# Performance work log

Measured on AMD Instinct MI355X. Metric: run time of the kernel, lower is better.

Reference implementation:

```python
import jax, jax.numpy as jnp
import numpy as np

D_K = 64
NEG_INF = -1.0e9


def setup_inputs() -> dict:
    key = jax.random.key(0)
    kq, kk, kv = jax.random.split(key, 3)
    B, H, S, D = 2, 16, 2048, D_K
    Q = jax.random.normal(kq, (B, H, S, D), dtype=jnp.float32)
    K = jax.random.normal(kk, (B, H, S, D), dtype=jnp.float32)
    V = jax.random.normal(kv, (B, H, S, D), dtype=jnp.float32)
    # causal mask: True where attention is DISALLOWED (strict upper triangle)
    attn_mask = jnp.triu(jnp.ones((S, S), dtype=bool), k=1)
    return {"Q": Q, "K": K, "V": V, "attn_mask": attn_mask}


def reference(Q, K, V, attn_mask):
    # scores = Q @ (K / sqrt(d_k))^T  -> [B,H,S,S]
    scale = 1.0 / np.sqrt(D_K).astype(np.float32)
    scores = jnp.einsum("bhqd,bhkd->bhqk", Q, K * scale)
    scores = jnp.where(attn_mask, NEG_INF, scores)  # masked_fill_(mask, -1e9)
    attn = jax.nn.softmax(scores, axis=-1)
    context = jnp.einsum("bhqk,bhkd->bhqd", attn, V)
    return (context, attn)
```

## Files before the change

kernel.cpp:

```cpp
#include <hip/hip_runtime.h>

constexpr int S_LEN = 2048;
constexpr int D_K   = 64;
constexpr int N_BH  = 32;
constexpr int KB    = 64;

typedef __attribute__((ext_vector_type(8))) short short8;
typedef __attribute__((ext_vector_type(4))) float f32x4;
typedef unsigned short ushort_t;

__device__ __forceinline__ unsigned short f2bf(float f) {
    unsigned int u = __builtin_bit_cast(unsigned int, f);
    u += 0x7fffu + ((u >> 16) & 1u);
    return (unsigned short)(u >> 16);
}
__device__ __forceinline__ float bf2f(unsigned short h) {
    unsigned int u = ((unsigned int)h) << 16;
    return __builtin_bit_cast(float, u);
}

__global__ __launch_bounds__(256)
void prep_k(const float* __restrict__ K, ushort_t* __restrict__ Kws) {
    const int idx = blockIdx.x * 256 + threadIdx.x;
    const float4* src = (const float4*)K + (size_t)idx * 2;
    float4 a = src[0], b = src[1];
    float x[8] = {a.x, a.y, a.z, a.w, b.x, b.y, b.z, b.w};
    short8 o;
    #pragma unroll
    for (int j = 0; j < 8; ++j) o[j] = (short)f2bf(x[j] * 0.125f);
    *(short8*)(Kws + (size_t)idx * 8) = o;
}

__global__ __launch_bounds__(256)
void prep_v(const float* __restrict__ V, ushort_t* __restrict__ Vws) {
    const int gid = blockIdx.x * 256 + threadIdx.x;
    const int u   = gid & 511;
    const int bc  = gid >> 9;
    const int c   = bc & 31;
    const int bh  = bc >> 5;
    const int kg  = u >> 6;
    const int d   = u & 63;
    const float* vp = V + ((size_t)bh * S_LEN + c * KB + kg * 8) * D_K + d;
    short8 o;
    #pragma unroll
    for (int i = 0; i < 8; ++i) o[i] = (short)f2bf(vp[(size_t)i * D_K]);
    *(short8*)(Vws + ((size_t)(bh * 32 + c) * D_K + d) * KB + kg * 8) = o;
}

__global__ __launch_bounds__(256, 4)
void sdpa_main(const float* __restrict__ Q, const ushort_t* __restrict__ Kws,
               const ushort_t* __restrict__ Vws, float* __restrict__ out)
{
    __shared__ __align__(16) ushort_t Kbuf[2][4096];
    __shared__ __align__(16) ushort_t Vbuf[2][4096];
    __shared__ __align__(16) ushort_t Plds[4][1024];

    const int tid = threadIdx.x;
    const int w   = tid >> 6;
    const int l   = tid & 63;
    const int lr  = l & 15;
    const int lh  = l >> 4;

    const int bx  = blockIdx.x;
    const int g   = bx >> 8;
    const int idx = bx & 255;
    const int bh  = idx >> 3;
    const int r   = idx & 7;
    int t;
    switch (g) {
        case 0:  t = 31 - r; break;
        case 1:  t = 16 + r; break;
        case 2:  t = 15 - r; break;
        default: t = r;      break;
    }
    const int nch = t + 1;
    const int q0  = t * 64;
    const int qg_base = q0 + w * 16 + lh * 4;

    float* ctx_out  = out;
    float* attn_out = out + (size_t)N_BH * S_LEN * D_K;

    const short8* Kt  = (const short8*)(Kws + (size_t)bh * S_LEN * D_K);
    const short8* Vt8 = (const short8*)(Vws + (size_t)bh * 32 * 4096);

    const int wrow0  = tid >> 3;
    const int wcol   = (tid & 7) << 4;
    const int wphys0 = wrow0 * 128 + (wcol ^ ((wrow0 & 7) << 4));
    const int wphys1 = wphys0 + 32 * 128;
    const int rsw    = (lr & 7) << 4;

    short8 qhi[2], qlo[2];
    {
        const float* qrow = Q + ((size_t)bh * S_LEN + q0 + w * 16 + lr) * D_K;
        #pragma unroll
        for (int ds = 0; ds < 2; ++ds) {
            const float4* p4 = (const float4*)(qrow + ds * 32 + lh * 8);
            float4 a = p4[0], bq = p4[1];
            float x[8] = {a.x, a.y, a.z, a.w, bq.x, bq.y, bq.z, bq.w};
            short8 hi, lo;
            #pragma unroll
            for (int j = 0; j < 8; ++j) {
                unsigned short h = f2bf(x[j]);
                hi[j] = (short)h;
                lo[j] = (short)f2bf(x[j] - bf2f(h));
            }
            qhi[ds] = hi; qlo[ds] = lo;
        }
    }

    float inv_[4];
    {
        float sum[4] = {0.f, 0.f, 0.f, 0.f};

        auto p1 = [&](const char* Kb, int c) {
            #pragma unroll
            for (int nt = 0; nt < 4; ++nt) {
                f32x4 acc = {0.f, 0.f, 0.f, 0.f};
                #pragma unroll
                for (int ks = 0; ks < 2; ++ks) {
                    short8 bk = *(const short8*)(Kb + (nt * 16 + lr) * 128 + ((ks * 64 + lh * 16) ^ rsw));
                    acc = __builtin_amdgcn_mfma_f32_16x16x32_bf16(qhi[ks], bk, acc, 0, 0, 0);
                }
                const int kg = c * KB + nt * 16 + lr;
                #pragma unroll
                for (int rr = 0; rr < 4; ++rr)
                    if (kg <= qg_base + rr) sum[rr] += __expf(fminf(acc[rr], 60.f));
            }
        };

        short8 kE0 = Kt[tid], kE1 = Kt[tid + 256];
        *(short8*)((char*)&Kbuf[0][0] + wphys0) = kE0;
        *(short8*)((char*)&Kbuf[0][0] + wphys1) = kE1;
        short8 kO0 = Kt[512 + tid], kO1 = Kt[512 + tid + 256];
        __syncthreads();
        for (int c = 0; c < nch; c += 2) {
            if (c + 2 < nch) { kE0 = Kt[(c + 2) * 512 + tid]; kE1 = Kt[(c + 2) * 512 + tid + 256]; }
            p1((const char*)&Kbuf[0][0], c);
            if (c + 1 < nch) {
                *(short8*)((char*)&Kbuf[1][0] + wphys0) = kO0;
                *(short8*)((char*)&Kbuf[1][0] + wphys1) = kO1;
            }
            __syncthreads();
            if (c + 1 < nch) {
                if (c + 3 < nch) { kO0 = Kt[(c + 3) * 512 + tid]; kO1 = Kt[(c + 3) * 512 + tid + 256]; }
                p1((const char*)&Kbuf[1][0], c + 1);
                if (c + 2 < nch) {
                    *(short8*)((char*)&Kbuf[0][0] + wphys0) = kE0;
                    *(short8*)((char*)&Kbuf[0][0] + wphys1) = kE1;
                }
                __syncthreads();
            }
        }
        #pragma unroll
        for (int rr = 0; rr < 4; ++rr) {
            float s = sum[rr];
            s += __shfl_xor(s, 1);
            s += __shfl_xor(s, 2);
            s += __shfl_xor(s, 4);
            s += __shfl_xor(s, 8);
            inv_[rr] = 1.f / s;
        }
    }

    f32x4 ctx[4];
    #pragma unroll
    for (int nt = 0; nt < 4; ++nt) ctx[nt] = (f32x4){0.f, 0.f, 0.f, 0.f};

    {
        auto p2 = [&](const char* Kb, const char* Vb, int c) {
            #pragma unroll
            for (int nt = 0; nt < 4; ++nt) {
                f32x4 acc = {0.f, 0.f, 0.f, 0.f};
                #pragma unroll
                for (int ks = 0; ks < 2; ++ks) {
                    short8 bk = *(const short8*)(Kb + (nt * 16 + lr) * 128 + ((ks * 64 + lh * 16) ^ rsw));
                    acc = __builtin_amdgcn_mfma_f32_16x16x32_bf16(qhi[ks], bk, acc, 0, 0, 0);
                    acc = __builtin_amdgcn_mfma_f32_16x16x32_bf16(qlo[ks], bk, acc, 0, 0, 0);
                }
                const int kg = c * KB + nt * 16 + lr;
                #pragma unroll
                for (int rr = 0; rr < 4; ++rr) {
                    const int pwr = lh * 4 + rr;
                    const int qg  = qg_base + rr;
                    float p = (kg <= qg) ? __expf(fminf(acc[rr], 60.f)) * inv_[rr] : 0.f;
                    attn_out[((size_t)bh * S_LEN + qg) * S_LEN + kg] = p;
                    Plds[w][pwr * 64 + ((nt * 16 + lr) ^ ((pwr & 7) << 3))] = f2bf(p);
                }
            }
            #pragma unroll
            for (int ks = 0; ks < 2; ++ks) {
                short8 pa = *(const short8*)&Plds[w][lr * 64 + ((ks * 32 + lh * 8) ^ ((lr & 7) << 3))];
                #pragma unroll
                for (int nt = 0; nt < 4; ++nt) {
                    short8 vb = *(const short8*)(Vb + (nt * 16 + lr) * 128 + ((ks * 64 + lh * 16) ^ rsw));
                    ctx[nt] = __builtin_amdgcn_mfma_f32_16x16x32_bf16(pa, vb, ctx[nt], 0, 0, 0);
                }
            }
        };

        short8 kE0 = Kt[tid],        kE1 = Kt[tid + 256];
        short8 vE0 = Vt8[tid],       vE1 = Vt8[tid + 256];
        *(short8*)((char*)&Kbuf[0][0] + wphys0) = kE0;
        *(short8*)((char*)&Kbuf[0][0] + wphys1) = kE1;
        *(short8*)((char*)&Vbuf[0][0] + wphys0) = vE0;
        *(short8*)((char*)&Vbuf[0][0] + wphys1) = vE1;
        short8 kO0 = Kt[512 + tid],  kO1 = Kt[512 + tid + 256];
        short8 vO0 = Vt8[512 + tid], vO1 = Vt8[512 + tid + 256];
        __syncthreads();
        for (int c = 0; c < nch; c += 2) {
            if (c + 2 < nch) {
                kE0 = Kt[(c + 2) * 512 + tid];  kE1 = Kt[(c + 2) * 512 + tid + 256];
                vE0 = Vt8[(c + 2) * 512 + tid]; vE1 = Vt8[(c + 2) * 512 + tid + 256];
            }
            p2((const char*)&Kbuf[0][0], (const char*)&Vbuf[0][0], c);
            if (c + 1 < nch) {
                *(short8*)((char*)&Kbuf[1][0] + wphys0) = kO0;
                *(short8*)((char*)&Kbuf[1][0] + wphys1) = kO1;
                *(short8*)((char*)&Vbuf[1][0] + wphys0) = vO0;
                *(short8*)((char*)&Vbuf[1][0] + wphys1) = vO1;
            }
            __syncthreads();
            if (c + 1 < nch) {
                if (c + 3 < nch) {
                    kO0 = Kt[(c + 3) * 512 + tid];  kO1 = Kt[(c + 3) * 512 + tid + 256];
                    vO0 = Vt8[(c + 3) * 512 + tid]; vO1 = Vt8[(c + 3) * 512 + tid + 256];
                }
                p2((const char*)&Kbuf[1][0], (const char*)&Vbuf[1][0], c + 1);
                if (c + 2 < nch) {
                    *(short8*)((char*)&Kbuf[0][0] + wphys0) = kE0;
                    *(short8*)((char*)&Kbuf[0][0] + wphys1) = kE1;
                    *(short8*)((char*)&Vbuf[0][0] + wphys0) = vE0;
                    *(short8*)((char*)&Vbuf[0][0] + wphys1) = vE1;
                }
                __syncthreads();
            }
        }
    }

    #pragma unroll
    for (int nt = 0; nt < 4; ++nt)
        #pragma unroll
        for (int rr = 0; rr < 4; ++rr)
            ctx_out[((size_t)bh * S_LEN + qg_base + rr) * D_K + nt * 16 + lr] = ctx[nt][rr];

    const int k0 = nch * KB;
    if (k0 < S_LEN) {
        const float4 z = {0.f, 0.f, 0.f, 0.f};
        float* rowp = attn_out + ((size_t)bh * S_LEN + q0 + (tid >> 2)) * S_LEN;
        for (int k = k0 + (tid & 3) * 4; k < S_LEN; k += 16)
            *(float4*)(rowp + k) = z;
    }
}

constexpr int LDP = 72;

__global__ __launch_bounds__(256)
void sdpa_fused_v1(const float* __restrict__ Q, const float* __restrict__ K,
                   const float* __restrict__ V, float* __restrict__ out)
{
    __shared__ __align__(16) unsigned short Klds[KB * LDP];
    __shared__ __align__(16) unsigned short Vtlds[D_K * LDP];
    __shared__ __align__(16) unsigned short Pl[4][16 * LDP];

    const int tid = threadIdx.x;
    const int w   = tid >> 6;
    const int l   = tid & 63;
    const int lr  = l & 15;
    const int lh  = l >> 4;

    const int bh   = blockIdx.y;
    const int qblk = (int)gridDim.x - 1 - (int)blockIdx.x;
    const int q0   = qblk * 64;
    const int qw   = q0 + w * 16;
    const int nchunks = qblk + 1;

    const size_t in_base = (size_t)bh * S_LEN * D_K;
    float* ctx_out  = out;
    float* attn_out = out + (size_t)N_BH * S_LEN * D_K;

    short8 qhi[2], qlo[2];
    {
        const float* qrow = Q + in_base + (size_t)(qw + lr) * D_K;
        #pragma unroll
        for (int ds = 0; ds < 2; ++ds) {
            const float4* p4 = (const float4*)(qrow + ds * 32 + lh * 8);
            float4 a = p4[0], b = p4[1];
            float x[8] = {a.x, a.y, a.z, a.w, b.x, b.y, b.z, b.w};
            short8 hi, lo;
            #pragma unroll
            for (int j = 0; j < 8; ++j) {
                unsigned short h = f2bf(x[j]);
                hi[j] = (short)h;
                lo[j] = (short)f2bf(x[j] - bf2f(h));
            }
            qhi[ds] = hi; qlo[ds] = lo;
        }
    }

    const int srow = tid >> 2;
    const int scol = (tid & 3) * 16;
    const float* kstage = K + in_base + (size_t)srow * D_K + scol;
    const float* vstage = V + in_base + (size_t)srow * D_K + scol;

    float inv_[4];
    {
        float sum[4] = {0.f, 0.f, 0.f, 0.f};
        for (int c = 0; c < nchunks; ++c) {
            {
                const float4* kp = (const float4*)(kstage + (size_t)c * KB * D_K);
                float4 a0 = kp[0], a1 = kp[1], a2 = kp[2], a3 = kp[3];
                float x[16] = {a0.x,a0.y,a0.z,a0.w, a1.x,a1.y,a1.z,a1.w,
                               a2.x,a2.y,a2.z,a2.w, a3.x,a3.y,a3.z,a3.w};
                short8 w0, w1;
                #pragma unroll
                for (int j = 0; j < 8; ++j) {
                    w0[j] = (short)f2bf(x[j]     * 0.125f);
                    w1[j] = (short)f2bf(x[j + 8] * 0.125f);
                }
                *(short8*)&Klds[srow * LDP + scol]     = w0;
                *(short8*)&Klds[srow * LDP + scol + 8] = w1;
            }
            __syncthreads();
            #pragma unroll
            for (int nt = 0; nt < 4; ++nt) {
                f32x4 acc = {0.f, 0.f, 0.f, 0.f};
                #pragma unroll
                for (int ks = 0; ks < 2; ++ks) {
                    short8 bk = *(const short8*)&Klds[(nt*16 + lr) * LDP + ks*32 + lh*8];
                    acc = __builtin_amdgcn_mfma_f32_16x16x32_bf16(qhi[ks], bk, acc, 0, 0, 0);
                    acc = __builtin_amdgcn_mfma_f32_16x16x32_bf16(qlo[ks], bk, acc, 0, 0, 0);
                }
                const int kg = c * KB + nt * 16 + lr;
                #pragma unroll
                for (int rr = 0; rr < 4; ++rr) {
                    if (kg <= qw + lh * 4 + rr)
                        sum[rr] += __expf(fminf(acc[rr], 60.f));
                }
            }
            __syncthreads();
        }
        #pragma unroll
        for (int rr = 0; rr < 4; ++rr) {
            float t = sum[rr];
            t += __shfl_xor(t, 1);
            t += __shfl_xor(t, 2);
            t += __shfl_xor(t, 4);
            t += __shfl_xor(t, 8);
            inv_[rr] = 1.f / t;
        }
    }

    f32x4 ctx[4];
    #pragma unroll
    for (int nt = 0; nt < 4; ++nt) ctx[nt] = (f32x4){0.f, 0.f, 0.f, 0.f};

    for (int c = 0; c < nchunks; ++c) {
        {
            const float4* kp = (const float4*)(kstage + (size_t)c * KB * D_K);
            float4 a0 = kp[0], a1 = kp[1], a2 = kp[2], a3 = kp[3];
            float x[16] = {a0.x,a0.y,a0.z,a0.w, a1.x,a1.y,a1.z,a1.w,
                           a2.x,a2.y,a2.z,a2.w, a3.x,a3.y,a3.z,a3.w};
            short8 w0, w1;
            #pragma unroll
            for (int j = 0; j < 8; ++j) {
                w0[j] = (short)f2bf(x[j]     * 0.125f);
                w1[j] = (short)f2bf(x[j + 8] * 0.125f);
            }
            *(short8*)&Klds[srow * LDP + scol]     = w0;
            *(short8*)&Klds[srow * LDP + scol + 8] = w1;

            const float4* vp = (const float4*)(vstage + (size_t)c * KB * D_K);
            float4 b0 = vp[0], b1 = vp[1], b2 = vp[2], b3 = vp[3];
            float y[16] = {b0.x,b0.y,b0.z,b0.w, b1.x,b1.y,b1.z,b1.w,
                           b2.x,b2.y,b2.z,b2.w, b3.x,b3.y,b3.z,b3.w};
            #pragma unroll
            for (int j = 0; j < 16; ++j)
                Vtlds[(scol + j) * LDP + srow] = f2bf(y[j]);
        }
        __syncthreads();

        #pragma unroll
        for (int nt = 0; nt < 4; ++nt) {
            f32x4 acc = {0.f, 0.f, 0.f, 0.f};
            #pragma unroll
            for (int ks = 0; ks < 2; ++ks) {
                short8 bk = *(const short8*)&Klds[(nt*16 + lr) * LDP + ks*32 + lh*8];
                acc = __builtin_amdgcn_mfma_f32_16x16x32_bf16(qhi[ks], bk, acc, 0, 0, 0);
                acc = __builtin_amdgcn_mfma_f32_16x16x32_bf16(qlo[ks], bk, acc, 0, 0, 0);
            }
            const int kg = c * KB + nt * 16 + lr;
            #pragma unroll
            for (int rr = 0; rr < 4; ++rr) {
                const int qg = qw + lh * 4 + rr;
                float p = (kg <= qg) ? __expf(fminf(acc[rr], 60.f)) * inv_[rr] : 0.f;
                attn_out[((size_t)bh * S_LEN + qg) * S_LEN + kg] = p;
                Pl[w][(lh * 4 + rr) * LDP + nt * 16 + lr] = f2bf(p);
            }
        }
        __syncthreads();

        #pragma unroll
        for (int ks = 0; ks < 2; ++ks) {
            short8 pa = *(const short8*)&Pl[w][lr * LDP + ks*32 + lh*8];
            #pragma unroll
            for (int nt = 0; nt < 4; ++nt) {
                short8 vb = *(const short8*)&Vtlds[(nt*16 + lr) * LDP + ks*32 + lh*8];
                ctx[nt] = __builtin_amdgcn_mfma_f32_16x16x32_bf16(pa, vb, ctx[nt], 0, 0, 0);
            }
        }
        __syncthreads();
    }

    #pragma unroll
    for (int nt = 0; nt < 4; ++nt)
        #pragma unroll
        for (int rr = 0; rr < 4; ++rr)
            ctx_out[((size_t)bh * S_LEN + qw + lh * 4 + rr) * D_K + nt * 16 + lr] = ctx[nt][rr];

    const int k0 = nchunks * KB;
    if (k0 < S_LEN) {
        const float4 z = {0.f, 0.f, 0.f, 0.f};
        for (int rr = 0; rr < 64; ++rr) {
            float* rowp = attn_out + ((size_t)bh * S_LEN + q0 + rr) * S_LEN;
            for (int k = k0 + tid * 4; k < S_LEN; k += 256 * 4)
                *(float4*)(rowp + k) = z;
        }
    }
}

extern "C" void kernel_launch(void* const* d_in, const int* in_sizes, int n_in,
                              void* d_out, int out_size, void* d_ws, size_t ws_size,
                              hipStream_t stream)
{
    const float* Q = (const float*)d_in[0];
    const float* K = (const float*)d_in[1];
    const float* V = (const float*)d_in[2];
    float* out = (float*)d_out;

    const size_t ws_needed = (size_t)2 * N_BH * S_LEN * D_K * sizeof(ushort_t);
    if (ws_size >= ws_needed) {
        ushort_t* Kws = (ushort_t*)d_ws;
        ushort_t* Vws = Kws + (size_t)N_BH * S_LEN * D_K;
        prep_k<<<2048, 256, 0, stream>>>(K, Kws);
        prep_v<<<2048, 256, 0, stream>>>(V, Vws);
        sdpa_main<<<1024, 256, 0, stream>>>(Q, Kws, Vws, out);
    } else {
        dim3 grid(S_LEN / 64, N_BH);
        sdpa_fused_v1<<<grid, 256, 0, stream>>>(Q, K, V, out);
    }
}
```

Measured before the change: 200.9 us.

## Use persistent blocks with atomic work queue for longest-first causal tile scheduling

```diff
diff --git a/kernel.cpp b/kernel.cpp
--- a/kernel.cpp
+++ b/kernel.cpp
@@ -49,11 +49,13 @@
 
 __global__ __launch_bounds__(256, 4)
 void sdpa_main(const float* __restrict__ Q, const ushort_t* __restrict__ Kws,
-               const ushort_t* __restrict__ Vws, float* __restrict__ out)
+               const ushort_t* __restrict__ Vws, float* __restrict__ out,
+               unsigned int* __restrict__ counter)
 {
     __shared__ __align__(16) ushort_t Kbuf[2][4096];
     __shared__ __align__(16) ushort_t Vbuf[2][4096];
     __shared__ __align__(16) ushort_t Plds[4][1024];
+    __shared__ int wk;
 
     const int tid = threadIdx.x;
     const int w   = tid >> 6;
@@ -61,27 +63,8 @@
     const int lr  = l & 15;
     const int lh  = l >> 4;
 
-    const int bx  = blockIdx.x;
-    const int g   = bx >> 8;
-    const int idx = bx & 255;
-    const int bh  = idx >> 3;
-    const int r   = idx & 7;
-    int t;
-    switch (g) {
-        case 0:  t = 31 - r; break;
-        case 1:  t = 16 + r; break;
-        case 2:  t = 15 - r; break;
-        default: t = r;      break;
-    }
-    const int nch = t + 1;
-    const int q0  = t * 64;
-    const int qg_base = q0 + w * 16 + lh * 4;
-
     float* ctx_out  = out;
     float* attn_out = out + (size_t)N_BH * S_LEN * D_K;
-
-    const short8* Kt  = (const short8*)(Kws + (size_t)bh * S_LEN * D_K);
-    const short8* Vt8 = (const short8*)(Vws + (size_t)bh * 32 * 4096);
 
     const int wrow0  = tid >> 3;
     const int wcol   = (tid & 7) << 4;
@@ -89,166 +72,188 @@
     const int wphys1 = wphys0 + 32 * 128;
     const int rsw    = (lr & 7) << 4;
 
-    short8 qhi[2], qlo[2];
-    {
-        const float* qrow = Q + ((size_t)bh * S_LEN + q0 + w * 16 + lr) * D_K;
-        #pragma unroll
-        for (int ds = 0; ds < 2; ++ds) {
-            const float4* p4 = (const float4*)(qrow + ds * 32 + lh * 8);
-            float4 a = p4[0], bq = p4[1];
-            float x[8] = {a.x, a.y, a.z, a.w, bq.x, bq.y, bq.z, bq.w};
-            short8 hi, lo;
-            #pragma unroll
-            for (int j = 0; j < 8; ++j) {
-                unsigned short h = f2bf(x[j]);
-                hi[j] = (short)h;
-                lo[j] = (short)f2bf(x[j] - bf2f(h));
-            }
-            qhi[ds] = hi; qlo[ds] = lo;
-        }
-    }
-
-    float inv_[4];
-    {
-        float sum[4] = {0.f, 0.f, 0.f, 0.f};
-
-        auto p1 = [&](const char* Kb, int c) {
-            #pragma unroll
-            for (int nt = 0; nt < 4; ++nt) {
-                f32x4 acc = {0.f, 0.f, 0.f, 0.f};
+    for (;;) {
+        if (tid == 0) wk = (int)atomicAdd(counter, 1u);
+        __syncthreads();
+        const int my = wk;
+        __syncthreads();
+        if (my >= 1024) break;
+
+        const int t  = 31 - (my >> 5);
+        const int bh = my & 31;
+        const int nch = t + 1;
+        const int q0  = t * 64;
+        const int qg_base = q0 + w * 16 + lh * 4;
+
+        const short8* Kt  = (const short8*)(Kws + (size_t)bh * S_LEN * D_K);
+        const short8* Vt8 = (const short8*)(Vws + (size_t)bh * 32 * 4096);
+
+        short8 qhi[2], qlo[2];
+        {
+            const float* qrow = Q + ((size_t)bh * S_LEN + q0 + w * 16 + lr) * D_K;
+            #pragma unroll
+            for (int ds = 0; ds < 2; ++ds) {
+                const float4* p4 = (const float4*)(qrow + ds * 32 + lh * 8);
+                float4 a = p4[0], bq = p4[1];
+                float x[8] = {a.x, a.y, a.z, a.w, bq.x, bq.y, bq.z, bq.w};
+                short8 hi, lo;
+                #pragma unroll
+                for (int j = 0; j < 8; ++j) {
+                    unsigned short h = f2bf(x[j]);
+                    hi[j] = (short)h;
+                    lo[j] = (short)f2bf(x[j] - bf2f(h));
+                }
+                qhi[ds] = hi; qlo[ds] = lo;
+            }
+        }
+
+        float inv_[4];
+        {
+            float sum[4] = {0.f, 0.f, 0.f, 0.f};
+
+            auto p1 = [&](const char* Kb, int c) {
+                #pragma unroll
+                for (int nt = 0; nt < 4; ++nt) {
+                    f32x4 acc = {0.f, 0.f, 0.f, 0.f};
+                    #pragma unroll
+                    for (int ks = 0; ks < 2; ++ks) {
+                        short8 bk = *(const short8*)(Kb + (nt * 16 + lr) * 128 + ((ks * 64 + lh * 16) ^ rsw));
+                        acc = __builtin_amdgcn_mfma_f32_16x16x32_bf16(qhi[ks], bk, acc, 0, 0, 0);
+                    }
+                    const int kg = c * KB + nt * 16 + lr;
+                    #pragma unroll
+                    for (int rr = 0; rr < 4; ++rr)
+                        if (kg <= qg_base + rr) sum[rr] += __expf(fminf(acc[rr], 60.f));
+                }
+            };
+
+            short8 kE0 = Kt[tid], kE1 = Kt[tid + 256];
+            *(short8*)((char*)&Kbuf[0][0] + wphys0) = kE0;
+            *(short8*)((char*)&Kbuf[0][0] + wphys1) = kE1;
+            short8 kO0, kO1;
+            if (nch > 1) { kO0 = Kt[512 + tid]; kO1 = Kt[512 + tid + 256]; }
+            __syncthreads();
+            for (int c = 0; c < nch; c += 2) {
+                if (c + 2 < nch) { kE0 = Kt[(c + 2) * 512 + tid]; kE1 = Kt[(c + 2) * 512 + tid + 256]; }
+                p1((const char*)&Kbuf[0][0], c);
+                if (c + 1 < nch) {
+                    *(short8*)((char*)&Kbuf[1][0] + wphys0) = kO0;
+                    *(short8*)((char*)&Kbuf[1][0] + wphys1) = kO1;
+                }
+                __syncthreads();
+                if (c + 1 < nch) {
+                    if (c + 3 < nch) { kO0 = Kt[(c + 3) * 512 + tid]; kO1 = Kt[(c + 3) * 512 + tid + 256]; }
+                    p1((const char*)&Kbuf[1][0], c + 1);
+                    if (c + 2 < nch) {
+                        *(short8*)((char*)&Kbuf[0][0] + wphys0) = kE0;
+                        *(short8*)((char*)&Kbuf[0][0] + wphys1) = kE1;
+                    }
+                    __syncthreads();
+                }
+            }
+            #pragma unroll
+            for (int rr = 0; rr < 4; ++rr) {
+                float s = sum[rr];
+                s += __shfl_xor(s, 1);
+                s += __shfl_xor(s, 2);
+                s += __shfl_xor(s, 4);
+                s += __shfl_xor(s, 8);
+                inv_[rr] = 1.f / s;
+            }
+        }
+
+        f32x4 ctx[4];
+        #pragma unroll
+        for (int nt = 0; nt < 4; ++nt) ctx[nt] = (f32x4){0.f, 0.f, 0.f, 0.f};
+
+        {
+            auto p2 = [&](const char* Kb, const char* Vb, int c) {
+                #pragma unroll
+                for (int nt = 0; nt < 4; ++nt) {
+                    f32x4 acc = {0.f, 0.f, 0.f, 0.f};
+                    #pragma unroll
+                    for (int ks = 0; ks < 2; ++ks) {
+                        short8 bk = *(const short8*)(Kb + (nt * 16 + lr) * 128 + ((ks * 64 + lh * 16) ^ rsw));
+                        acc = __builtin_amdgcn_mfma_f32_16x16x32_bf16(qhi[ks], bk, acc, 0, 0, 0);
+                        acc = __builtin_amdgcn_mfma_f32_16x16x32_bf16(qlo[ks], bk, acc, 0, 0, 0);
+                    }
+                    const int kg = c * KB + nt * 16 + lr;
+                    #pragma unroll
+                    for (int rr = 0; rr < 4; ++rr) {
+                        const int pwr = lh * 4 + rr;
+                        const int qg  = qg_base + rr;
+                        float p = (kg <= qg) ? __expf(fminf(acc[rr], 60.f)) * inv_[rr] : 0.f;
+                        attn_out[((size_t)bh * S_LEN + qg) * S_LEN + kg] = p;
+                        Plds[w][pwr * 64 + ((nt * 16 + lr) ^ ((pwr & 7) << 3))] = f2bf(p);
+                    }
+                }
                 #pragma unroll
                 for (int ks = 0; ks < 2; ++ks) {
-                    short8 bk = *(const short8*)(Kb + (nt * 16 + lr) * 128 + ((ks * 64 + lh * 16) ^ rsw));
-                    acc = __builtin_amdgcn_mfma_f32_16x16x32_bf16(qhi[ks], bk, acc, 0, 0, 0);
-                }
-                const int kg = c * KB + nt * 16 + lr;
-                #pragma unroll
-                for (int rr = 0; rr < 4; ++rr)
-                    if (kg <= qg_base + rr) sum[rr] += __expf(fminf(acc[rr], 60.f));
-            }
-        };
-
-        short8 kE0 = Kt[tid], kE1 = Kt[tid + 256];
-        *(short8*)((char*)&Kbuf[0][0] + wphys0) = kE0;
-        *(short8*)((char*)&Kbuf[0][0] + wphys1) = kE1;
-        short8 kO0 = Kt[512 + tid], kO1 = Kt[512 + tid + 256];
-        __syncthreads();
-        for (int c = 0; c < nch; c += 2) {
-            if (c + 2 < nch) { kE0 = Kt[(c + 2) * 512 + tid]; kE1 = Kt[(c + 2) * 512 + tid + 256]; }
-            p1((const char*)&Kbuf[0][0], c);
-            if (c + 1 < nch) {
-                *(short8*)((char*)&Kbuf[1][0] + wphys0) = kO0;
-                *(short8*)((char*)&Kbuf[1][0] + wphys1) = kO1;
+                    short8 pa = *(const short8*)&Plds[w][lr * 64 + ((ks * 32 + lh * 8) ^ ((lr & 7) << 3))];
+                    #pragma unroll
+                    for (int nt = 0; nt < 4; ++nt) {
+                        short8 vb = *(const short8*)(Vb + (nt * 16 + lr) * 128 + ((ks * 64 + lh * 16) ^ rsw));
+                        ctx[nt] = __builtin_amdgcn_mfma_f32_16x16x32_bf16(pa, vb, ctx[nt], 0, 0, 0);
+                    }
+                }
+            };
+
+            short8 kE0 = Kt[tid],        kE1 = Kt[tid + 256];
+            short8 vE0 = Vt8[tid],       vE1 = Vt8[tid + 256];
+            *(short8*)((char*)&Kbuf[0][0] + wphys0) = kE0;
+            *(short8*)((char*)&Kbuf[0][0] + wphys1) = kE1;
+            *(short8*)((char*)&Vbuf[0][0] + wphys0) = vE0;
+            *(short8*)((char*)&Vbuf[0][0] + wphys1) = vE1;
+            short8 kO0, kO1, vO0, vO1;
+            if (nch > 1) {
+                kO0 = Kt[512 + tid];  kO1 = Kt[512 + tid + 256];
+                vO0 = Vt8[512 + tid]; vO1 = Vt8[512 + tid + 256];
             }
             __syncthreads();
-            if (c + 1 < nch) {
-                if (c + 3 < nch) { kO0 = Kt[(c + 3) * 512 + tid]; kO1 = Kt[(c + 3) * 512 + tid + 256]; }
-                p1((const char*)&Kbuf[1][0], c + 1);
+            for (int c = 0; c < nch; c += 2) {
                 if (c + 2 < nch) {
-                    *(short8*)((char*)&Kbuf[0][0] + wphys0) = kE0;
-                    *(short8*)((char*)&Kbuf[0][0] + wphys1) = kE1;
+                    kE0 = Kt[(c + 2) * 512 + tid];  kE1 = Kt[(c + 2) * 512 + tid + 256];
+                    vE0 = Vt8[(c + 2) * 512 + tid]; vE1 = Vt8[(c + 2) * 512 + tid + 256];
+                }
+                p2((const char*)&Kbuf[0][0], (const char*)&Vbuf[0][0], c);
+                if (c + 1 < nch) {
+                    *(short8*)((char*)&Kbuf[1][0] + wphys0) = kO0;
+                    *(short8*)((char*)&Kbuf[1][0] + wphys1) = kO1;
+                    *(short8*)((char*)&Vbuf[1][0] + wphys0) = vO0;
+                    *(short8*)((char*)&Vbuf[1][0] + wphys1) = vO1;
                 }
                 __syncthreads();
-            }
-        }
-        #pragma unroll
-        for (int rr = 0; rr < 4; ++rr) {
-            float s = sum[rr];
-            s += __shfl_xor(s, 1);
-            s += __shfl_xor(s, 2);
-            s += __shfl_xor(s, 4);
-            s += __shfl_xor(s, 8);
-            inv_[rr] = 1.f / s;
-        }
-    }
-
-    f32x4 ctx[4];
-    #pragma unroll
-    for (int nt = 0; nt < 4; ++nt) ctx[nt] = (f32x4){0.f, 0.f, 0.f, 0.f};
-
-    {
-        auto p2 = [&](const char* Kb, const char* Vb, int c) {
-            #pragma unroll
-            for (int nt = 0; nt < 4; ++nt) {
-                f32x4 acc = {0.f, 0.f, 0.f, 0.f};
-                #pragma unroll
-                for (int ks = 0; ks < 2; ++ks) {
-                    short8 bk = *(const short8*)(Kb + (nt * 16 + lr) * 128 + ((ks * 64 + lh * 16) ^ rsw));
-                    acc = __builtin_amdgcn_mfma_f32_16x16x32_bf16(qhi[ks], bk, acc, 0, 0, 0);
-                    acc = __builtin_amdgcn_mfma_f32_16x16x32_bf16(qlo[ks], bk, acc, 0, 0, 0);
-                }
-                const int kg = c * KB + nt * 16 + lr;
-                #pragma unroll
-                for (int rr = 0; rr < 4; ++rr) {
-                    const int pwr = lh * 4 + rr;
-                    const int qg  = qg_base + rr;
-                    float p = (kg <= qg) ? __expf(fminf(acc[rr], 60.f)) * inv_[rr] : 0.f;
-                    attn_out[((size_t)bh * S_LEN + qg) * S_LEN + kg] = p;
-                    Plds[w][pwr * 64 + ((nt * 16 + lr) ^ ((pwr & 7) << 3))] = f2bf(p);
-                }
-            }
-            #pragma unroll
-            for (int ks = 0; ks < 2; ++ks) {
-                short8 pa = *(const short8*)&Plds[w][lr * 64 + ((ks * 32 + lh * 8) ^ ((lr & 7) << 3))];
-                #pragma unroll
-                for (int nt = 0; nt < 4; ++nt) {
-                    short8 vb = *(const short8*)(Vb + (nt * 16 + lr) * 128 + ((ks * 64 + lh * 16) ^ rsw));
-                    ctx[nt] = __builtin_amdgcn_mfma_f32_16x16x32_bf16(pa, vb, ctx[nt], 0, 0, 0);
-                }
-            }
-        };
-
-        short8 kE0 = Kt[tid],        kE1 = Kt[tid + 256];
-        short8 vE0 = Vt8[tid],       vE1 = Vt8[tid + 256];
-        *(short8*)((char*)&Kbuf[0][0] + wphys0) = kE0;
-        *(short8*)((char*)&Kbuf[0][0] + wphys1) = kE1;
-        *(short8*)((char*)&Vbuf[0][0] + wphys0) = vE0;
-        *(short8*)((char*)&Vbuf[0][0] + wphys1) = vE1;
-        short8 kO0 = Kt[512 + tid],  kO1 = Kt[512 + tid + 256];
-        short8 vO0 = Vt8[512 + tid], vO1 = Vt8[512 + tid + 256];
-        __syncthreads();
-        for (int c = 0; c < nch; c += 2) {
-            if (c + 2 < nch) {
-                kE0 = Kt[(c + 2) * 512 + tid];  kE1 = Kt[(c + 2) * 512 + tid + 256];
-                vE0 = Vt8[(c + 2) * 512 + tid]; vE1 = Vt8[(c + 2) * 512 + tid + 256];
-            }
-            p2((const char*)&Kbuf[0][0], (const char*)&Vbuf[0][0], c);
-            if (c + 1 < nch) {
-                *(short8*)((char*)&Kbuf[1][0] + wphys0) = kO0;
-                *(short8*)((char*)&Kbuf[1][0] + wphys1) = kO1;
-                *(short8*)((char*)&Vbuf[1][0] + wphys0) = vO0;
-                *(short8*)((char*)&Vbuf[1][0] + wphys1) = vO1;
-            }
-            __syncthreads();
-            if (c + 1 < nch) {
-                if (c + 3 < nch) {
-                    kO0 = Kt[(c + 3) * 512 + tid];  kO1 = Kt[(c + 3) * 512 + tid + 256];
-                    vO0 = Vt8[(c + 3) * 512 + tid]; vO1 = Vt8[(c + 3) * 512 + tid + 256];
-                }
-                p2((const char*)&Kbuf[1][0], (const char*)&Vbuf[1][0], c + 1);
-                if (c + 2 < nch) {
-                    *(short8*)((char*)&Kbuf[0][0] + wphys0) = kE0;
-                    *(short8*)((char*)&Kbuf[0][0] + wphys1) = kE1;
-                    *(short8*)((char*)&Vbuf[0][0] + wphys0) = vE0;
-                    *(short8*)((char*)&Vbuf[0][0] + wphys1) = vE1;
-                }
-                __syncthreads();
-            }
-        }
-    }
-
-    #pragma unroll
-    for (int nt = 0; nt < 4; ++nt)
-        #pragma unroll
-        for (int rr = 0; rr < 4; ++rr)
-            ctx_out[((size_t)bh * S_LEN + qg_base + rr) * D_K + nt * 16 + lr] = ctx[nt][rr];
-
-    const int k0 = nch * KB;
-    if (k0 < S_LEN) {
-        const float4 z = {0.f, 0.f, 0.f, 0.f};
-        float* rowp = attn_out + ((size_t)bh * S_LEN + q0 + (tid >> 2)) * S_LEN;
-        for (int k = k0 + (tid & 3) * 4; k < S_LEN; k += 16)
-            *(float4*)(rowp + k) = z;
+                if (c + 1 < nch) {
+                    if (c + 3 < nch) {
+                        kO0 = Kt[(c + 3) * 512 + tid];  kO1 = Kt[(c + 3) * 512 + tid + 256];
+                        vO0 = Vt8[(c + 3) * 512 + tid]; vO1 = Vt8[(c + 3) * 512 + tid + 256];
+                    }
+                    p2((const char*)&Kbuf[1][0], (const char*)&Vbuf[1][0], c + 1);
+                    if (c + 2 < nch) {
+                        *(short8*)((char*)&Kbuf[0][0] + wphys0) = kE0;
+                        *(short8*)((char*)&Kbuf[0][0] + wphys1) = kE1;
+                        *(short8*)((char*)&Vbuf[0][0] + wphys0) = vE0;
+                        *(short8*)((char*)&Vbuf[0][0] + wphys1) = vE1;
+                    }
+                    __syncthreads();
+                }
+            }
+        }
+
+        #pragma unroll
+        for (int nt = 0; nt < 4; ++nt)
+            #pragma unroll
+            for (int rr = 0; rr < 4; ++rr)
+                ctx_out[((size_t)bh * S_LEN + qg_base + rr) * D_K + nt * 16 + lr] = ctx[nt][rr];
+
+        const int k0 = nch * KB;
+        if (k0 < S_LEN) {
+            const float4 z = {0.f, 0.f, 0.f, 0.f};
+            float* rowp = attn_out + ((size_t)bh * S_LEN + q0 + (tid >> 2)) * S_LEN;
+            for (int k = k0 + (tid & 3) * 4; k < S_LEN; k += 16)
+                *(float4*)(rowp + k) = z;
+        }
+        __syncthreads();
     }
 }
 
@@ -437,13 +442,16 @@
     const float* V = (const float*)d_in[2];
     float* out = (float*)d_out;
 
-    const size_t ws_needed = (size_t)2 * N_BH * S_LEN * D_K * sizeof(ushort_t);
+    const size_t kv_bytes   = (size_t)2 * N_BH * S_LEN * D_K * sizeof(ushort_t);
+    const size_t ws_needed  = kv_bytes + 256;
     if (ws_size >= ws_needed) {
         ushort_t* Kws = (ushort_t*)d_ws;
         ushort_t* Vws = Kws + (size_t)N_BH * S_LEN * D_K;
+        unsigned int* counter = (unsigned int*)((char*)d_ws + kv_bytes);
+        hipMemsetAsync(counter, 0, sizeof(unsigned int), stream);
         prep_k<<<2048, 256, 0, stream>>>(K, Kws);
         prep_v<<<2048, 256, 0, stream>>>(V, Vws);
-        sdpa_main<<<1024, 256, 0, stream>>>(Q, Kws, Vws, out);
+        sdpa_main<<<768, 256, 0, stream>>>(Q, Kws, Vws, out, counter);
     } else {
         dim3 grid(S_LEN / 64, N_BH);
         sdpa_fused_v1<<<grid, 256, 0, stream>>>(Q, K, V, out);
```

Result: slower. 209.3 us (+4.2%).

## Process two adjacent query tiles per block, fusing tile B's sum pass into A

Applied to the files above, without the earlier changes.

```diff
diff --git a/kernel.cpp b/kernel.cpp
--- a/kernel.cpp
+++ b/kernel.cpp
@@ -61,21 +61,15 @@
     const int lr  = l & 15;
     const int lh  = l >> 4;
 
-    const int bx  = blockIdx.x;
-    const int g   = bx >> 8;
-    const int idx = bx & 255;
-    const int bh  = idx >> 3;
-    const int r   = idx & 7;
-    int t;
-    switch (g) {
-        case 0:  t = 31 - r; break;
-        case 1:  t = 16 + r; break;
-        case 2:  t = 15 - r; break;
-        default: t = r;      break;
-    }
-    const int nch = t + 1;
-    const int q0  = t * 64;
-    const int qg_base = q0 + w * 16 + lh * 4;
+    const int b   = blockIdx.x;
+    const int p   = b >> 5;
+    const int bh  = b & 31;
+    const int nchB = 2 * p + 1;
+    const int nchA = 2 * p + 2;
+    const int q0B  = (2 * p) * 64;
+    const int q0A  = (2 * p + 1) * 64;
+    const int qgA  = q0A + w * 16 + lh * 4;
+    const int qgB  = q0B + w * 16 + lh * 4;
 
     float* ctx_out  = out;
     float* attn_out = out + (size_t)N_BH * S_LEN * D_K;
@@ -89,42 +83,51 @@
     const int wphys1 = wphys0 + 32 * 128;
     const int rsw    = (lr & 7) << 4;
 
-    short8 qhi[2], qlo[2];
-    {
-        const float* qrow = Q + ((size_t)bh * S_LEN + q0 + w * 16 + lr) * D_K;
+    short8 qhiA[2], qloA[2], qhiB[2];
+    {
+        const float* qrowA = Q + ((size_t)bh * S_LEN + q0A + w * 16 + lr) * D_K;
+        const float* qrowB = Q + ((size_t)bh * S_LEN + q0B + w * 16 + lr) * D_K;
         #pragma unroll
         for (int ds = 0; ds < 2; ++ds) {
-            const float4* p4 = (const float4*)(qrow + ds * 32 + lh * 8);
-            float4 a = p4[0], bq = p4[1];
-            float x[8] = {a.x, a.y, a.z, a.w, bq.x, bq.y, bq.z, bq.w};
+            const float4* pa = (const float4*)(qrowA + ds * 32 + lh * 8);
+            float4 a0 = pa[0], a1 = pa[1];
+            float xa[8] = {a0.x, a0.y, a0.z, a0.w, a1.x, a1.y, a1.z, a1.w};
             short8 hi, lo;
             #pragma unroll
             for (int j = 0; j < 8; ++j) {
-                unsigned short h = f2bf(x[j]);
+                unsigned short h = f2bf(xa[j]);
                 hi[j] = (short)h;
-                lo[j] = (short)f2bf(x[j] - bf2f(h));
-            }
-            qhi[ds] = hi; qlo[ds] = lo;
-        }
-    }
-
-    float inv_[4];
+                lo[j] = (short)f2bf(xa[j] - bf2f(h));
+            }
+            qhiA[ds] = hi; qloA[ds] = lo;
+
+            const float4* pb = (const float4*)(qrowB + ds * 32 + lh * 8);
+            float4 b0 = pb[0], b1 = pb[1];
+            float xb[8] = {b0.x, b0.y, b0.z, b0.w, b1.x, b1.y, b1.z, b1.w};
+            short8 hb;
+            #pragma unroll
+            for (int j = 0; j < 8; ++j) hb[j] = (short)f2bf(xb[j]);
+            qhiB[ds] = hb;
+        }
+    }
+
+    float invA[4];
     {
         float sum[4] = {0.f, 0.f, 0.f, 0.f};
 
-        auto p1 = [&](const char* Kb, int c) {
+        auto p1A = [&](const char* Kb, int c) {
             #pragma unroll
             for (int nt = 0; nt < 4; ++nt) {
                 f32x4 acc = {0.f, 0.f, 0.f, 0.f};
                 #pragma unroll
                 for (int ks = 0; ks < 2; ++ks) {
                     short8 bk = *(const short8*)(Kb + (nt * 16 + lr) * 128 + ((ks * 64 + lh * 16) ^ rsw));
-                    acc = __builtin_amdgcn_mfma_f32_16x16x32_bf16(qhi[ks], bk, acc, 0, 0, 0);
+                    acc = __builtin_amdgcn_mfma_f32_16x16x32_bf16(qhiA[ks], bk, acc, 0, 0, 0);
                 }
                 const int kg = c * KB + nt * 16 + lr;
                 #pragma unroll
                 for (int rr = 0; rr < 4; ++rr)
-                    if (kg <= qg_base + rr) sum[rr] += __expf(fminf(acc[rr], 60.f));
+                    if (kg <= qgA + rr) sum[rr] += __expf(fminf(acc[rr], 60.f));
             }
         };
 
@@ -133,18 +136,18 @@
         *(short8*)((char*)&Kbuf[0][0] + wphys1) = kE1;
         short8 kO0 = Kt[512 + tid], kO1 = Kt[512 + tid + 256];
         __syncthreads();
-        for (int c = 0; c < nch; c += 2) {
-            if (c + 2 < nch) { kE0 = Kt[(c + 2) * 512 + tid]; kE1 = Kt[(c + 2) * 512 + tid + 256]; }
-            p1((const char*)&Kbuf[0][0], c);
-            if (c + 1 < nch) {
+        for (int c = 0; c < nchA; c += 2) {
+            if (c + 2 < nchA) { kE0 = Kt[(c + 2) * 512 + tid]; kE1 = Kt[(c + 2) * 512 + tid + 256]; }
+            p1A((const char*)&Kbuf[0][0], c);
+            if (c + 1 < nchA) {
                 *(short8*)((char*)&Kbuf[1][0] + wphys0) = kO0;
                 *(short8*)((char*)&Kbuf[1][0] + wphys1) = kO1;
             }
             __syncthreads();
-            if (c + 1 < nch) {
-                if (c + 3 < nch) { kO0 = Kt[(c + 3) * 512 + tid]; kO1 = Kt[(c + 3) * 512 + tid + 256]; }
-                p1((const char*)&Kbuf[1][0], c + 1);
-                if (c + 2 < nch) {
+            if (c + 1 < nchA) {
+                if (c + 3 < nchA) { kO0 = Kt[(c + 3) * 512 + tid]; kO1 = Kt[(c + 3) * 512 + tid + 256]; }
+                p1A((const char*)&Kbuf[1][0], c + 1);
+                if (c + 2 < nchA) {
                     *(short8*)((char*)&Kbuf[0][0] + wphys0) = kE0;
                     *(short8*)((char*)&Kbuf[0][0] + wphys1) = kE1;
                 }
@@ -158,33 +161,34 @@
             s += __shfl_xor(s, 2);
             s += __shfl_xor(s, 4);
             s += __shfl_xor(s, 8);
-            inv_[rr] = 1.f / s;
+            invA[rr] = 1.f / s;
         }
     }
 
     f32x4 ctx[4];
     #pragma unroll
     for (int nt = 0; nt < 4; ++nt) ctx[nt] = (f32x4){0.f, 0.f, 0.f, 0.f};
-
-    {
-        auto p2 = [&](const char* Kb, const char* Vb, int c) {
+    float sumB[4] = {0.f, 0.f, 0.f, 0.f};
+
+    {
+        auto mid = [&](const char* Kb, const char* Vb, int c) {
             #pragma unroll
             for (int nt = 0; nt < 4; ++nt) {
                 f32x4 acc = {0.f, 0.f, 0.f, 0.f};
                 #pragma unroll
                 for (int ks = 0; ks < 2; ++ks) {
                     short8 bk = *(const short8*)(Kb + (nt * 16 + lr) * 128 + ((ks * 64 + lh * 16) ^ rsw));
-                    acc = __builtin_amdgcn_mfma_f32_16x16x32_bf16(qhi[ks], bk, acc, 0, 0, 0);
-                    acc = __builtin_amdgcn_mfma_f32_16x16x32_bf16(qlo[ks], bk, acc, 0, 0, 0);
+                    acc = __builtin_amdgcn_mfma_f32_16x16x32_bf16(qhiA[ks], bk, acc, 0, 0, 0);
+                    acc = __builtin_amdgcn_mfma_f32_16x16x32_bf16(qloA[ks], bk, acc, 0, 0, 0);
                 }
                 const int kg = c * KB + nt * 16 + lr;
                 #pragma unroll
                 for (int rr = 0; rr < 4; ++rr) {
                     const int pwr = lh * 4 + rr;
-                    const int qg  = qg_base + rr;
-                    float p = (kg <= qg) ? __expf(fminf(acc[rr], 60.f)) * inv_[rr] : 0.f;
-                    attn_out[((size_t)bh * S_LEN + qg) * S_LEN + kg] = p;
-                    Plds[w][pwr * 64 + ((nt * 16 + lr) ^ ((pwr & 7) << 3))] = f2bf(p);
+                    const int qg  = qgA + rr;
+                    float pv = (kg <= qg) ? __expf(fminf(acc[rr], 60.f)) * invA[rr] : 0.f;
+                    attn_out[((size_t)bh * S_LEN + qg) * S_LEN + kg] = pv;
+                    Plds[w][pwr * 64 + ((nt * 16 + lr) ^ ((pwr & 7) << 3))] = f2bf(pv);
                 }
             }
             #pragma unroll
@@ -194,6 +198,21 @@
                 for (int nt = 0; nt < 4; ++nt) {
                     short8 vb = *(const short8*)(Vb + (nt * 16 + lr) * 128 + ((ks * 64 + lh * 16) ^ rsw));
                     ctx[nt] = __builtin_amdgcn_mfma_f32_16x16x32_bf16(pa, vb, ctx[nt], 0, 0, 0);
+                }
+            }
+            if (c < nchB) {
+                #pragma unroll
+                for (int nt = 0; nt < 4; ++nt) {
+                    f32x4 acc = {0.f, 0.f, 0.f, 0.f};
+                    #pragma unroll
+                    for (int ks = 0; ks < 2; ++ks) {
+                        short8 bk = *(const short8*)(Kb + (nt * 16 + lr) * 128 + ((ks * 64 + lh * 16) ^ rsw));
+                        acc = __builtin_amdgcn_mfma_f32_16x16x32_bf16(qhiB[ks], bk, acc, 0, 0, 0);
+                    }
+                    const int kg = c * KB + nt * 16 + lr;
+                    #pragma unroll
+                    for (int rr = 0; rr < 4; ++rr)
+                        if (kg <= qgB + rr) sumB[rr] += __expf(fminf(acc[rr], 60.f));
                 }
             }
         };
@@ -207,26 +226,26 @@
         short8 kO0 = Kt[512 + tid],  kO1 = Kt[512 + tid + 256];
         short8 vO0 = Vt8[512 + tid], vO1 = Vt8[512 + tid + 256];
         __syncthreads();
-        for (int c = 0; c < nch; c += 2) {
-            if (c + 2 < nch) {
+        for (int c = 0; c < nchA; c += 2) {
+            if (c + 2 < nchA) {
                 kE0 = Kt[(c + 2) * 512 + tid];  kE1 = Kt[(c + 2) * 512 + tid + 256];
                 vE0 = Vt8[(c + 2) * 512 + tid]; vE1 = Vt8[(c + 2) * 512 + tid + 256];
             }
-            p2((const char*)&Kbuf[0][0], (const char*)&Vbuf[0][0], c);
-            if (c + 1 < nch) {
+            mid((const char*)&Kbuf[0][0], (const char*)&Vbuf[0][0], c);
+            if (c + 1 < nchA) {
                 *(short8*)((char*)&Kbuf[1][0] + wphys0) = kO0;
                 *(short8*)((char*)&Kbuf[1][0] + wphys1) = kO1;
                 *(short8*)((char*)&Vbuf[1][0] + wphys0) = vO0;
                 *(short8*)((char*)&Vbuf[1][0] + wphys1) = vO1;
             }
             __syncthreads();
-            if (c + 1 < nch) {
-                if (c + 3 < nch) {
+            if (c + 1 < nchA) {
+                if (c + 3 < nchA) {
                     kO0 = Kt[(c + 3) * 512 + tid];  kO1 = Kt[(c + 3) * 512 + tid + 256];
                     vO0 = Vt8[(c + 3) * 512 + tid]; vO1 = Vt8[(c + 3) * 512 + tid + 256];
                 }
-                p2((const char*)&Kbuf[1][0], (const char*)&Vbuf[1][0], c + 1);
-                if (c + 2 < nch) {
+                mid((const char*)&Kbuf[1][0], (const char*)&Vbuf[1][0], c + 1);
+                if (c + 2 < nchA) {
                     *(short8*)((char*)&Kbuf[0][0] + wphys0) = kE0;
                     *(short8*)((char*)&Kbuf[0][0] + wphys1) = kE1;
                     *(short8*)((char*)&Vbuf[0][0] + wphys0) = vE0;
@@ -241,14 +260,133 @@
     for (int nt = 0; nt < 4; ++nt)
         #pragma unroll
         for (int rr = 0; rr < 4; ++rr)
-            ctx_out[((size_t)bh * S_LEN + qg_base + rr) * D_K + nt * 16 + lr] = ctx[nt][rr];
-
-    const int k0 = nch * KB;
-    if (k0 < S_LEN) {
+            ctx_out[((size_t)bh * S_LEN + qgA + rr) * D_K + nt * 16 + lr] = ctx[nt][rr];
+
+    float invB[4];
+    #pragma unroll
+    for (int rr = 0; rr < 4; ++rr) {
+        float s = sumB[rr];
+        s += __shfl_xor(s, 1);
+        s += __shfl_xor(s, 2);
+        s += __shfl_xor(s, 4);
+        s += __shfl_xor(s, 8);
+        invB[rr] = 1.f / s;
+    }
+    short8 qloB[2];
+    {
+        const float* qrowB = Q + ((size_t)bh * S_LEN + q0B + w * 16 + lr) * D_K;
+        #pragma unroll
+        for (int ds = 0; ds < 2; ++ds) {
+            const float4* pb = (const float4*)(qrowB + ds * 32 + lh * 8);
+            float4 b0 = pb[0], b1 = pb[1];
+            float xb[8] = {b0.x, b0.y, b0.z, b0.w, b1.x, b1.y, b1.z, b1.w};
+            short8 lo;
+            #pragma unroll
+            for (int j = 0; j < 8; ++j) {
+                unsigned short h = f2bf(xb[j]);
+                lo[j] = (short)f2bf(xb[j] - bf2f(h));
+            }
+            qloB[ds] = lo;
+        }
+    }
+
+    #pragma unroll
+    for (int nt = 0; nt < 4; ++nt) ctx[nt] = (f32x4){0.f, 0.f, 0.f, 0.f};
+
+    {
+        auto p2B = [&](const char* Kb, const char* Vb, int c) {
+            #pragma unroll
+            for (int nt = 0; nt < 4; ++nt) {
+                f32x4 acc = {0.f, 0.f, 0.f, 0.f};
+                #pragma unroll
+                for (int ks = 0; ks < 2; ++ks) {
+                    short8 bk = *(const short8*)(Kb + (nt * 16 + lr) * 128 + ((ks * 64 + lh * 16) ^ rsw));
+                    acc = __builtin_amdgcn_mfma_f32_16x16x32_bf16(qhiB[ks], bk, acc, 0, 0, 0);
+                    acc = __builtin_amdgcn_mfma_f32_16x16x32_bf16(qloB[ks], bk, acc, 0, 0, 0);
+                }
+                const int kg = c * KB + nt * 16 + lr;
+                #pragma unroll
+                for (int rr = 0; rr < 4; ++rr) {
+                    const int pwr = lh * 4 + rr;
+                    const int qg  = qgB + rr;
+                    float pv = (kg <= qg) ? __expf(fminf(acc[rr], 60.f)) * invB[rr] : 0.f;
+                    attn_out[((size_t)bh * S_LEN + qg) * S_LEN + kg] = pv;
+                    Plds[w][pwr * 64 + ((nt * 16 + lr) ^ ((pwr & 7) << 3))] = f2bf(pv);
+                }
+            }
+            #pragma unroll
+            for (int ks = 0; ks < 2; ++ks) {
+                short8 pa = *(const short8*)&Plds[w][lr * 64 + ((ks * 32 + lh * 8) ^ ((lr & 7) << 3))];
+                #pragma unroll
+                for (int nt = 0; nt < 4; ++nt) {
+                    short8 vb = *(const short8*)(Vb + (nt * 16 + lr) * 128 + ((ks * 64 + lh * 16) ^ rsw));
+                    ctx[nt] = __builtin_amdgcn_mfma_f32_16x16x32_bf16(pa, vb, ctx[nt], 0, 0, 0);
+                }
+            }
+        };
+
+        short8 kE0 = Kt[tid],        kE1 = Kt[tid + 256];
+        short8 vE0 = Vt8[tid],       vE1 = Vt8[tid + 256];
+        *(short8*)((char*)&Kbuf[0][0] + wphys0) = kE0;
+        *(short8*)((char*)&Kbuf[0][0] + wphys1) = kE1;
+        *(short8*)((char*)&Vbuf[0][0] + wphys0) = vE0;
+        *(short8*)((char*)&Vbuf[0][0] + wphys1) = vE1;
+        short8 kO0, kO1, vO0, vO1;
+        if (nchB > 1) {
+            kO0 = Kt[512 + tid];  kO1 = Kt[512 + tid + 256];
+            vO0 = Vt8[512 + tid]; vO1 = Vt8[512 + tid + 256];
+        }
+        __syncthreads();
+        for (int c = 0; c < nchB; c += 2) {
+            if (c + 2 < nchB) {
+                kE0 = Kt[(c + 2) * 512 + tid];  kE1 = Kt[(c + 2) * 512 + tid + 256];
+                vE0 = Vt8[(c + 2) * 512 + tid]; vE1 = Vt8[(c + 2) * 512 + tid + 256];
+            }
+            p2B((const char*)&Kbuf[0][0], (const char*)&Vbuf[0][0], c);
+            if (c + 1 < nchB) {
+                *(short8*)((char*)&Kbuf[1][0] + wphys0) = kO0;
+                *(short8*)((char*)&Kbuf[1][0] + wphys1) = kO1;
+                *(short8*)((char*)&Vbuf[1][0] + wphys0) = vO0;
+                *(short8*)((char*)&Vbuf[1][0] + wphys1) = vO1;
+            }
+            __syncthreads();
+            if (c + 1 < nchB) {
+                if (c + 3 < nchB) {
+                    kO0 = Kt[(c + 3) * 512 + tid];  kO1 = Kt[(c + 3) * 512 + tid + 256];
+                    vO0 = Vt8[(c + 3) * 512 + tid]; vO1 = Vt8[(c + 3) * 512 + tid + 256];
+                }
+                p2B((const char*)&Kbuf[1][0], (const char*)&Vbuf[1][0], c + 1);
+                if (c + 2 < nchB) {
+                    *(short8*)((char*)&Kbuf[0][0] + wphys0) = kE0;
+                    *(short8*)((char*)&Kbuf[0][0] + wphys1) = kE1;
+                    *(short8*)((char*)&Vbuf[0][0] + wphys0) = vE0;
+                    *(short8*)((char*)&Vbuf[0][0] + wphys1) = vE1;
+                }
+                __syncthreads();
+            }
+        }
+    }
+
+    #pragma unroll
+    for (int nt = 0; nt < 4; ++nt)
+        #pragma unroll
+        for (int rr = 0; rr < 4; ++rr)
+            ctx_out[((size_t)bh * S_LEN + qgB + rr) * D_K + nt * 16 + lr] = ctx[nt][rr];
+
+    {
         const float4 z = {0.f, 0.f, 0.f, 0.f};
-        float* rowp = attn_out + ((size_t)bh * S_LEN + q0 + (tid >> 2)) * S_LEN;
-        for (int k = k0 + (tid & 3) * 4; k < S_LEN; k += 16)
-            *(float4*)(rowp + k) = z;
+        const int k0A = nchA * KB;
+        if (k0A < S_LEN) {
+            float* rowp = attn_out + ((size_t)bh * S_LEN + q0A + (tid >> 2)) * S_LEN;
+            for (int k = k0A + (tid & 3) * 4; k < S_LEN; k += 16)
+                *(float4*)(rowp + k) = z;
+        }
+        const int k0B = nchB * KB;
+        if (k0B < S_LEN) {
+            float* rowp = attn_out + ((size_t)bh * S_LEN + q0B + (tid >> 2)) * S_LEN;
+            for (int k = k0B + (tid & 3) * 4; k < S_LEN; k += 16)
+                *(float4*)(rowp + k) = z;
+        }
     }
 }
 
@@ -443,7 +581,7 @@
         ushort_t* Vws = Kws + (size_t)N_BH * S_LEN * D_K;
         prep_k<<<2048, 256, 0, stream>>>(K, Kws);
         prep_v<<<2048, 256, 0, stream>>>(V, Vws);
-        sdpa_main<<<1024, 256, 0, stream>>>(Q, Kws, Vws, out);
+        sdpa_main<<<512, 256, 0, stream>>>(Q, Kws, Vws, out);
     } else {
         dim3 grid(S_LEN / 64, N_BH);
         sdpa_fused_v1<<<grid, 256, 0, stream>>>(Q, K, V, out);
```

After: 348.7 us. 73.6% more time.
